# Optimization experiments

Hardware: AMD Instinct MI355X
Metric: run time of the kernel (lower is better)

The kernel has to match this reference:

```python
import jax, jax.numpy as jnp
import numpy as np

EPS = 1e-5
GROUPS = 8
HEADS = 8


def setup_inputs() -> dict:
    key = jax.random.key(0)
    k_x, k_qkv, k_out = jax.random.split(key, 3)
    B, C, X, Y, Z = 2, 256, 16, 16, 16
    x = jax.random.normal(k_x, (B, C, X, Y, Z), dtype=jnp.float32)
    norm_w = jnp.ones((C,), dtype=jnp.float32)
    norm_b = jnp.zeros((C,), dtype=jnp.float32)
    # 1x1 Conv3d weights stored as [out_ch, in_ch]
    w_qkv = jax.random.normal(k_qkv, (3 * C, C), dtype=jnp.float32) * (C ** -0.5)
    w_out = jax.random.normal(k_out, (C, C), dtype=jnp.float32) * (C ** -0.5)
    b_out = jnp.zeros((C,), dtype=jnp.float32)
    return {"x": x, "norm_w": norm_w, "norm_b": norm_b,
            "w_qkv": w_qkv, "w_out": w_out, "b_out": b_out}


def group_norm(x, w, b):
    B, C, X, Y, Z = x.shape
    xg = x.reshape(B, GROUPS, C // GROUPS, X, Y, Z)
    mean = xg.mean(axis=(2, 3, 4, 5), keepdims=True)
    var = xg.var(axis=(2, 3, 4, 5), keepdims=True)
    xn = ((xg - mean) * jax.lax.rsqrt(var + EPS)).reshape(B, C, X, Y, Z)
    return xn * w[None, :, None, None, None] + b[None, :, None, None, None]


def reference(x, norm_w, norm_b, w_qkv, w_out, b_out):
    B, C, X, Y, Z = x.shape
    H = HEADS
    D = C // H
    N = X * Y * Z
    scale = D ** -0.5

    xn = group_norm(x, norm_w, norm_b)
    # 1x1 conv QKV projection (bias=False): [B, 3C, X, Y, Z] flattened to tokens
    qkv = jnp.einsum('oc,bcn->bon', w_qkv, xn.reshape(B, C, N))
    q, k, v = jnp.split(qkv, 3, axis=1)            # each [B, C, N]
    q = q.reshape(B, H, D, N)
    k = k.reshape(B, H, D, N)
    v = v.reshape(B, H, D, N)

    scores = jnp.einsum('bhds,bhdt->bhst', q, k) * scale   # [B, H, N, N]
    probs = jax.nn.softmax(scores, axis=-1)
    out = jnp.einsum('bhst,bhdt->bhds', probs, v)          # [B, H, D, N]
    out = out.reshape(B, C, N)

    # 1x1 conv output projection (with bias)
    out = jnp.einsum('oc,bcn->bon', w_out, out) + b_out[None, :, None]
    return out.reshape(B, C, X, Y, Z) + x
```

## Files before the change

kernel.cpp:

```cpp
#include <hip/hip_runtime.h>

#define NB 2
#define NC 256
#define NT 4096
#define NG 8
#define NH 8
#define EPSV 1e-5f
#define SCALE_L2E 0.25503164427f
#define NCHUNK 4
#define CHTOK (NT / NCHUNK)
#define NIT (CHTOK / 32)
#define PO_ELEMS ((size_t)NB * NC * NT)

typedef __attribute__((ext_vector_type(8))) __bf16 bf16x8;
typedef __attribute__((ext_vector_type(8))) unsigned short u16x8;
typedef __attribute__((ext_vector_type(4))) unsigned short u16x4;
typedef __attribute__((ext_vector_type(4))) unsigned int u32x4;
typedef __attribute__((ext_vector_type(2))) unsigned int u32x2;
typedef __attribute__((ext_vector_type(4))) float f32x4;

static __device__ __forceinline__ unsigned short f2bf(float f) {
    union { float f; unsigned int u; } v; v.f = f;
    unsigned int r = v.u + 0x7fffu + ((v.u >> 16) & 1u);
    return (unsigned short)(r >> 16);
}
static __device__ __forceinline__ float bf2f(unsigned short u) {
    union { unsigned int u; float f; } v; v.u = ((unsigned int)u) << 16;
    return v.f;
}
static __device__ __forceinline__ bf16x8 ldbf8(const unsigned short* p) {
    u16x8 u = *(const u16x8*)p;
    return __builtin_bit_cast(bf16x8, u);
}
static __device__ __forceinline__ unsigned int cvtpk(float lo, float hi) {
    unsigned int d;
    asm("v_cvt_pk_bf16_f32 %0, %1, %2" : "=v"(d) : "v"(lo), "v"(hi));
    return d;
}

__global__ __launch_bounds__(256) void k_stats_partial(const float* __restrict__ x,
                                                       float* __restrict__ part) {
    int bg = blockIdx.x >> 5;
    int p  = blockIdx.x & 31;
    const float4* base = (const float4*)(x + (size_t)bg * 131072 + (size_t)p * 4096);
    float s = 0.f, s2 = 0.f;
#pragma unroll
    for (int i = 0; i < 4; ++i) {
        float4 v = base[threadIdx.x + i * 256];
        s  += v.x + v.y + v.z + v.w;
        s2 += v.x * v.x + v.y * v.y + v.z * v.z + v.w * v.w;
    }
    __shared__ float ss[256], sq[256];
    ss[threadIdx.x] = s; sq[threadIdx.x] = s2;
    __syncthreads();
    for (int off = 128; off > 0; off >>= 1) {
        if (threadIdx.x < off) {
            ss[threadIdx.x] += ss[threadIdx.x + off];
            sq[threadIdx.x] += sq[threadIdx.x + off];
        }
        __syncthreads();
    }
    if (threadIdx.x == 0) {
        part[blockIdx.x * 2 + 0] = ss[0];
        part[blockIdx.x * 2 + 1] = sq[0];
    }
}

__global__ __launch_bounds__(64) void k_stats_final(const float* __restrict__ part,
                                                    float* __restrict__ stats) {
    int bg = blockIdx.x;
    float s = 0.f, s2 = 0.f;
    if (threadIdx.x < 32) {
        s  = part[(bg * 32 + threadIdx.x) * 2 + 0];
        s2 = part[(bg * 32 + threadIdx.x) * 2 + 1];
    }
#pragma unroll
    for (int off = 16; off > 0; off >>= 1) {
        s  += __shfl_down(s, off);
        s2 += __shfl_down(s2, off);
    }
    if (threadIdx.x == 0) {
        const float inv = 1.0f / 131072.0f;
        float mean = s * inv;
        float var  = s2 * inv - mean * mean;
        stats[bg * 2 + 0] = mean;
        stats[bg * 2 + 1] = rsqrtf(var + EPSV);
    }
}

__global__ __launch_bounds__(256) void k_wprep2(const float* __restrict__ wq,
                                                const float* __restrict__ wo,
                                                unsigned short* __restrict__ wq_bf,
                                                unsigned short* __restrict__ wo_bf) {
    int bidx = blockIdx.x;
    const float* src;
    unsigned short* dst;
    int off;
    if (bidx < 96) { src = wq; dst = wq_bf; off = bidx * 2048; }
    else           { src = wo; dst = wo_bf; off = (bidx - 96) * 2048; }
    int idx = off + threadIdx.x * 8;
    float4 a = *(const float4*)(src + idx);
    float4 c = *(const float4*)(src + idx + 4);
    u32x4 o = { cvtpk(a.x, a.y), cvtpk(a.z, a.w),
                cvtpk(c.x, c.y), cvtpk(c.z, c.w) };
    *(u32x4*)(dst + idx) = o;
}

__global__ __launch_bounds__(256) void k_xprep(const float* __restrict__ x,
                                               const float* __restrict__ nw,
                                               const float* __restrict__ nbias,
                                               const float* __restrict__ stats,
                                               unsigned short* __restrict__ xnT) {
    __shared__ unsigned short T[64][72];
    int b = blockIdx.z, c0 = blockIdx.y * 64, n0 = blockIdx.x * 64;
    int tid = threadIdx.x;
    int c_l = tid >> 2, nq = (tid & 3) * 16;
    int c = c0 + c_l;
    int grp = c >> 5;
    float mean = stats[(b * NG + grp) * 2 + 0];
    float rstd = stats[(b * NG + grp) * 2 + 1];
    float wsc = nw[c] * rstd;
    float bb  = nbias[c] - mean * wsc;
    const float4* src = (const float4*)(x + ((size_t)(b * NC + c)) * NT + n0 + nq);
#pragma unroll
    for (int i = 0; i < 4; ++i) {
        float4 v = src[i];
        T[nq + i * 4 + 0][c_l] = f2bf(v.x * wsc + bb);
        T[nq + i * 4 + 1][c_l] = f2bf(v.y * wsc + bb);
        T[nq + i * 4 + 2][c_l] = f2bf(v.z * wsc + bb);
        T[nq + i * 4 + 3][c_l] = f2bf(v.w * wsc + bb);
    }
    __syncthreads();
    int n_l = tid >> 2, cq = (tid & 3) * 16;
    unsigned short* dst = xnT + ((size_t)b * NT + n0 + n_l) * 256 + c0 + cq;
    *(u16x8*)dst       = *(const u16x8*)&T[n_l][cq];
    *(u16x8*)(dst + 8) = *(const u16x8*)&T[n_l][cq + 8];
}

__global__ __launch_bounds__(256) void k_qkv_mfma(const unsigned short* __restrict__ wq_bf,
                                                  const unsigned short* __restrict__ xnT,
                                                  unsigned short* __restrict__ qkT,
                                                  unsigned short* __restrict__ vbf) {
    int b = blockIdx.z, o0 = blockIdx.y * 64, n0 = blockIdx.x * 64;
    int tid = threadIdx.x;
    int w = tid >> 6, lane = tid & 63, c16 = lane & 15, g = lane >> 4;
    int n_tok = n0 + w * 16 + c16;
    const unsigned short* Bsrc = xnT + ((size_t)b * NT + n_tok) * 256 + g * 8;
    const unsigned short* Asrc = wq_bf + (size_t)(o0 + c16) * 256 + g * 8;
    f32x4 acc[4] = {};
    for (int kk = 0; kk < 8; ++kk) {
        bf16x8 bfr = ldbf8(Bsrc + kk * 32);
#pragma unroll
        for (int ot = 0; ot < 4; ++ot) {
            bf16x8 afr = ldbf8(Asrc + ot * 16 * 256 + kk * 32);
            acc[ot] = __builtin_amdgcn_mfma_f32_16x16x32_bf16(afr, bfr, acc[ot], 0, 0, 0);
        }
    }
    if (o0 < 512) {
        int qk = o0 >> 8;
        float sc = (qk == 0) ? SCALE_L2E : 1.0f;
#pragma unroll
        for (int ot = 0; ot < 4; ++ot) {
            int ob = o0 + ot * 16 + g * 4;
            int h  = (ob >> 5) & 7;
            int d4 = ob & 31;
            unsigned int u0 = cvtpk(acc[ot][0] * sc, acc[ot][1] * sc);
            unsigned int u1 = cvtpk(acc[ot][2] * sc, acc[ot][3] * sc);
            u16x4 pk = { (unsigned short)(u0 & 0xFFFF), (unsigned short)(u0 >> 16),
                         (unsigned short)(u1 & 0xFFFF), (unsigned short)(u1 >> 16) };
            *(u16x4*)(qkT + ((((size_t)qk * NB + b) * NH + h) * NT + n_tok) * 32 + d4) = pk;
        }
    } else {
#pragma unroll
        for (int ot = 0; ot < 4; ++ot) {
            int ob = (o0 - 512) + ot * 16 + g * 4;
            int h = (ob >> 5) & 7;
            int d = ob & 31;
            unsigned short* dst = vbf + (((size_t)b * NH + h) * 32 + d) * NT + n_tok;
            dst[0]      = f2bf(acc[ot][0]);
            dst[NT]     = f2bf(acc[ot][1]);
            dst[2 * NT] = f2bf(acc[ot][2]);
            dst[3 * NT] = f2bf(acc[ot][3]);
        }
    }
}

__global__ __launch_bounds__(256) void k_attn(const unsigned short* __restrict__ qkT,
                                              const unsigned short* __restrict__ vbf,
                                              unsigned short* __restrict__ pO,
                                              float* __restrict__ pl) {
    __shared__ unsigned short KV[2048];
    __shared__ unsigned int Pd[4][640];
    int bid = blockIdx.x;
    int xcd  = bid & 7;
    int slot = bid >> 3;
    int combo = xcd * 8 + (slot >> 5);
    int sb    = slot & 31;
    int b  = combo >> 5;
    int ch = (combo >> 3) & 3;
    int h  = combo & 7;

    int tid = threadIdx.x;
    int w = tid >> 6, lane = tid & 63, col = lane & 15, g = lane >> 4;
    int s0 = sb * 128 + w * 32;

    const unsigned short* qB = qkT + ((((size_t)0 * NB + b) * NH + h) * NT) * 32;
    const unsigned short* kB = qkT + ((((size_t)1 * NB + b) * NH + h) * NT) * 32;
    const unsigned short* vB = vbf + (((size_t)b * NH + h) * 32) * NT;

    bf16x8 qf[2];
    qf[0] = ldbf8(qB + (size_t)(s0 + col) * 32 + g * 8);
    qf[1] = ldbf8(qB + (size_t)(s0 + 16 + col) * 32 + g * 8);

    u16x8 ou;
#pragma unroll
    for (int j = 0; j < 8; ++j) ou[j] = 0x3F80;
    const bf16x8 ones = __builtin_bit_cast(bf16x8, ou);

    const unsigned short* gs;
    int gstep;
    if (tid < 128) {
        gs = kB + ((size_t)ch * CHTOK) * 32 + tid * 8;
        gstep = 1024;
    } else {
        int idx = tid - 128;
        int d = idx >> 2, tq = (idx & 3) * 8;
        gs = vB + (size_t)d * NT + ch * CHTOK + tq;
        gstep = 32;
    }

    f32x4 oacc[2][2] = {};
    f32x4 lacc[2] = {};
    unsigned int* Pw = Pd[w];

    u16x8 stg = *(const u16x8*)gs;

    for (int it = 0; it < NIT; ++it) {
        __syncthreads();
        *(u16x8*)&KV[tid * 8] = stg;
        __syncthreads();
        if (it + 1 < NIT)
            stg = *(const u16x8*)(gs + (size_t)(it + 1) * gstep);
        bf16x8 k0 = ldbf8(&KV[0] + col * 32 + g * 8);
        bf16x8 k1 = ldbf8(&KV[0] + (16 + col) * 32 + g * 8);
        bf16x8 v0 = ldbf8(&KV[0] + 1024 + col * 32 + g * 8);
        bf16x8 v1 = ldbf8(&KV[0] + 1024 + (16 + col) * 32 + g * 8);
        const f32x4 z = {0.f, 0.f, 0.f, 0.f};
#pragma unroll
        for (int st = 0; st < 2; ++st) {
            int s_l = st * 16 + col;
            f32x4 sa = __builtin_amdgcn_mfma_f32_16x16x32_bf16(k0, qf[st], z, 0, 0, 0);
            f32x4 sb2 = __builtin_amdgcn_mfma_f32_16x16x32_bf16(k1, qf[st], z, 0, 0, 0);
            unsigned int W0 = cvtpk(__builtin_amdgcn_exp2f(sa[0]),
                                    __builtin_amdgcn_exp2f(sa[1]));
            unsigned int W1 = cvtpk(__builtin_amdgcn_exp2f(sa[2]),
                                    __builtin_amdgcn_exp2f(sa[3]));
            unsigned int W2 = cvtpk(__builtin_amdgcn_exp2f(sb2[0]),
                                    __builtin_amdgcn_exp2f(sb2[1]));
            unsigned int W3 = cvtpk(__builtin_amdgcn_exp2f(sb2[2]),
                                    __builtin_amdgcn_exp2f(sb2[3]));
            u32x2 wlo = {W0, W1};
            u32x2 whi = {W2, W3};
            *(u32x2*)&Pw[s_l * 20 + g * 2]     = wlo;
            *(u32x2*)&Pw[s_l * 20 + 8 + g * 2] = whi;
            u32x4 rv = *(const u32x4*)&Pw[s_l * 20 + g * 4];
            bf16x8 pf = __builtin_bit_cast(bf16x8, rv);
            lacc[st]    = __builtin_amdgcn_mfma_f32_16x16x32_bf16(ones, pf, lacc[st], 0, 0, 0);
            oacc[0][st] = __builtin_amdgcn_mfma_f32_16x16x32_bf16(v0, pf, oacc[0][st], 0, 0, 0);
            oacc[1][st] = __builtin_amdgcn_mfma_f32_16x16x32_bf16(v1, pf, oacc[1][st], 0, 0, 0);
        }
    }

    unsigned short* pOc = pO + (size_t)ch * PO_ELEMS;
#pragma unroll
    for (int dt = 0; dt < 2; ++dt)
#pragma unroll
        for (int st = 0; st < 2; ++st) {
            int s = s0 + st * 16 + col;
            unsigned int u0 = cvtpk(oacc[dt][st][0], oacc[dt][st][1]);
            unsigned int u1 = cvtpk(oacc[dt][st][2], oacc[dt][st][3]);
            u16x4 pk = { (unsigned short)(u0 & 0xFFFF), (unsigned short)(u0 >> 16),
                         (unsigned short)(u1 & 0xFFFF), (unsigned short)(u1 >> 16) };
            *(u16x4*)&pOc[((size_t)(b * NT + s)) * 256 + h * 32 + dt * 16 + g * 4] = pk;
        }
    if (g == 0) {
#pragma unroll
        for (int st = 0; st < 2; ++st) {
            int s = s0 + st * 16 + col;
            pl[(((size_t)ch * NB + b) * NH + h) * NT + s] = lacc[st][0];
        }
    }
}

__global__ __launch_bounds__(512) void k_out_fused(const unsigned short* __restrict__ pO,
                                                   const float* __restrict__ pl,
                                                   const unsigned short* __restrict__ wo_bf,
                                                   const float* __restrict__ bout,
                                                   const float* __restrict__ x,
                                                   float* __restrict__ out) {
    __shared__ unsigned short attL[32 * 264];
    int b = blockIdx.y, n0 = blockIdx.x * 32;
    int tid = threadIdx.x;

#pragma unroll
    for (int i = 0; i < 4; ++i) {
        int q = tid * 4 + i;
        int tok_l = q >> 6;
        int cq = (q & 63) * 4;
        int h = cq >> 5;
        int s = n0 + tok_l;
        float num[4] = {0.f, 0.f, 0.f, 0.f};
        float den = 0.f;
#pragma unroll
        for (int chn = 0; chn < NCHUNK; ++chn) {
            u16x4 ov = *(const u16x4*)&pO[(size_t)chn * PO_ELEMS +
                                          ((size_t)(b * NT + s)) * 256 + cq];
            den += pl[(((size_t)chn * NB + b) * NH + h) * NT + s];
            num[0] += bf2f(ov[0]); num[1] += bf2f(ov[1]);
            num[2] += bf2f(ov[2]); num[3] += bf2f(ov[3]);
        }
        float rd = 1.0f / den;
        u16x4 res = { f2bf(num[0] * rd), f2bf(num[1] * rd),
                      f2bf(num[2] * rd), f2bf(num[3] * rd) };
        *(u16x4*)&attL[tok_l * 264 + cq] = res;
    }
    __syncthreads();

    int w = tid >> 6, lane = tid & 63, c16 = lane & 15, g = lane >> 4;
    int tg = w & 1, og = w >> 1;
    int n_tok = n0 + tg * 16 + c16;
    int o0 = og * 64;
    const unsigned short* Bsrc = &attL[(tg * 16 + c16) * 264 + g * 8];
    const unsigned short* Asrc = wo_bf + (size_t)(o0 + c16) * 256 + g * 8;
    f32x4 acc[4] = {};
    for (int kk = 0; kk < 8; ++kk) {
        bf16x8 bfr = ldbf8(Bsrc + kk * 32);
#pragma unroll
        for (int ot = 0; ot < 4; ++ot) {
            bf16x8 afr = ldbf8(Asrc + ot * 16 * 256 + kk * 32);
            acc[ot] = __builtin_amdgcn_mfma_f32_16x16x32_bf16(afr, bfr, acc[ot], 0, 0, 0);
        }
    }
#pragma unroll
    for (int ot = 0; ot < 4; ++ot) {
        int ob = o0 + ot * 16 + g * 4;
#pragma unroll
        for (int rr = 0; rr < 4; ++rr) {
            int o = ob + rr;
            size_t off = ((size_t)(b * NC + o)) * NT + n_tok;
            out[off] = acc[ot][rr] + bout[o] + x[off];
        }
    }
}

extern "C" void kernel_launch(void* const* d_in, const int* in_sizes, int n_in,
                              void* d_out, int out_size, void* d_ws, size_t ws_size,
                              hipStream_t stream) {
    const float* x    = (const float*)d_in[0];
    const float* nw   = (const float*)d_in[1];
    const float* nb   = (const float*)d_in[2];
    const float* wqkv = (const float*)d_in[3];
    const float* wout = (const float*)d_in[4];
    const float* bout = (const float*)d_in[5];
    float* out = (float*)d_out;
    char* wsb = (char*)d_ws;

    unsigned short* qkT = (unsigned short*)wsb;
    unsigned short* vbf = (unsigned short*)(wsb + 8u * 1024 * 1024);
    unsigned short* pO  = (unsigned short*)(wsb + 12u * 1024 * 1024);
    float* pl   = (float*)(wsb + 28u * 1024 * 1024);
    float* part = (float*)(wsb + 29u * 1024 * 1024);
    float* stats = part + 1024;
    unsigned short* wo_bf = (unsigned short*)(wsb + 30u * 1024 * 1024);
    unsigned short* xnT   = pO;
    unsigned short* wq_bf = (unsigned short*)(wsb + 16u * 1024 * 1024);

    k_stats_partial<<<512, 256, 0, stream>>>(x, part);
    k_stats_final<<<16, 64, 0, stream>>>(part, stats);
    k_wprep2<<<128, 256, 0, stream>>>(wqkv, wout, wq_bf, wo_bf);
    k_xprep<<<dim3(NT / 64, NC / 64, NB), 256, 0, stream>>>(x, nw, nb, stats, xnT);
    k_qkv_mfma<<<dim3(NT / 64, 12, NB), 256, 0, stream>>>(wq_bf, xnT, qkT, vbf);
    k_attn<<<dim3(NB * NCHUNK * NH * 32), 256, 0, stream>>>(qkT, vbf, pO, pl);
    k_out_fused<<<dim3(128, NB), 512, 0, stream>>>(pO, pl, wo_bf, bout, x, out);
}
```

Measured before the change: 121.5 us.

## Keep softmax probabilities in registers by permuting V layout; pad LDS rows

Removes the per-wave LDS round trip that reshuffled the exp'd score fragments into MFMA B-operand layout. Instead, V is loaded from global in two 4-token halves and stored into LDS so its k-index ordering matches the score accumulator register layout, letting the packed probabilities feed the PV MFMA directly. K and V rows in LDS are padded to a stride of 40 to reduce bank conflicts. The register prefetch of the next tile is dropped, so global loads are no longer overlapped with compute, and V global loads become narrower 8-byte accesses.

```diff
diff --git a/kernel.cpp b/kernel.cpp
--- a/kernel.cpp
+++ b/kernel.cpp
@@ -189,8 +189,7 @@
                                               const unsigned short* __restrict__ vbf,
                                               unsigned short* __restrict__ pO,
                                               float* __restrict__ pl) {
-    __shared__ unsigned short KV[2048];
-    __shared__ unsigned int Pd[4][640];
+    __shared__ unsigned short KV[2560];
     int bid = blockIdx.x;
     int xcd  = bid & 7;
     int slot = bid >> 3;
@@ -217,38 +216,43 @@
     for (int j = 0; j < 8; ++j) ou[j] = 0x3F80;
     const bf16x8 ones = __builtin_bit_cast(bf16x8, ou);
 
-    const unsigned short* gs;
-    int gstep;
+    const unsigned short* gsK = kB;
+    const unsigned short* gsVA = vB;
+    const unsigned short* gsVB = vB;
+    int ldst = 0;
     if (tid < 128) {
-        gs = kB + ((size_t)ch * CHTOK) * 32 + tid * 8;
-        gstep = 1024;
+        gsK  = kB + ((size_t)ch * CHTOK) * 32 + tid * 8;
+        ldst = (tid >> 2) * 40 + (tid & 3) * 8;
     } else {
         int idx = tid - 128;
-        int d = idx >> 2, tq = (idx & 3) * 8;
-        gs = vB + (size_t)d * NT + ch * CHTOK + tq;
-        gstep = 32;
+        int d = idx >> 2, q = idx & 3;
+        gsVA = vB + (size_t)d * NT + ch * CHTOK + q * 4;
+        gsVB = gsVA + 16;
+        ldst = 1280 + d * 40 + q * 8;
     }
 
     f32x4 oacc[2][2] = {};
     f32x4 lacc[2] = {};
-    unsigned int* Pw = Pd[w];
-
-    u16x8 stg = *(const u16x8*)gs;
 
     for (int it = 0; it < NIT; ++it) {
         __syncthreads();
-        *(u16x8*)&KV[tid * 8] = stg;
+        if (tid < 128) {
+            *(u16x8*)&KV[ldst] = *(const u16x8*)(gsK + (size_t)it * 1024);
+        } else {
+            u16x4 va4 = *(const u16x4*)(gsVA + it * 32);
+            u16x4 vb4 = *(const u16x4*)(gsVB + it * 32);
+            u16x8 vv = { va4[0], va4[1], va4[2], va4[3],
+                         vb4[0], vb4[1], vb4[2], vb4[3] };
+            *(u16x8*)&KV[ldst] = vv;
+        }
         __syncthreads();
-        if (it + 1 < NIT)
-            stg = *(const u16x8*)(gs + (size_t)(it + 1) * gstep);
-        bf16x8 k0 = ldbf8(&KV[0] + col * 32 + g * 8);
-        bf16x8 k1 = ldbf8(&KV[0] + (16 + col) * 32 + g * 8);
-        bf16x8 v0 = ldbf8(&KV[0] + 1024 + col * 32 + g * 8);
-        bf16x8 v1 = ldbf8(&KV[0] + 1024 + (16 + col) * 32 + g * 8);
+        bf16x8 k0 = ldbf8(&KV[col * 40 + g * 8]);
+        bf16x8 k1 = ldbf8(&KV[(16 + col) * 40 + g * 8]);
+        bf16x8 v0 = ldbf8(&KV[1280 + col * 40 + g * 8]);
+        bf16x8 v1 = ldbf8(&KV[1280 + (16 + col) * 40 + g * 8]);
         const f32x4 z = {0.f, 0.f, 0.f, 0.f};
 #pragma unroll
         for (int st = 0; st < 2; ++st) {
-            int s_l = st * 16 + col;
             f32x4 sa = __builtin_amdgcn_mfma_f32_16x16x32_bf16(k0, qf[st], z, 0, 0, 0);
             f32x4 sb2 = __builtin_amdgcn_mfma_f32_16x16x32_bf16(k1, qf[st], z, 0, 0, 0);
             unsigned int W0 = cvtpk(__builtin_amdgcn_exp2f(sa[0]),
@@ -259,12 +263,8 @@
                                     __builtin_amdgcn_exp2f(sb2[1]));
             unsigned int W3 = cvtpk(__builtin_amdgcn_exp2f(sb2[2]),
                                     __builtin_amdgcn_exp2f(sb2[3]));
-            u32x2 wlo = {W0, W1};
-            u32x2 whi = {W2, W3};
-            *(u32x2*)&Pw[s_l * 20 + g * 2]     = wlo;
-            *(u32x2*)&Pw[s_l * 20 + 8 + g * 2] = whi;
-            u32x4 rv = *(const u32x4*)&Pw[s_l * 20 + g * 4];
-            bf16x8 pf = __builtin_bit_cast(bf16x8, rv);
+            u32x4 pbw = {W0, W1, W2, W3};
+            bf16x8 pf = __builtin_bit_cast(bf16x8, pbw);
             lacc[st]    = __builtin_amdgcn_mfma_f32_16x16x32_bf16(ones, pf, lacc[st], 0, 0, 0);
             oacc[0][st] = __builtin_amdgcn_mfma_f32_16x16x32_bf16(v0, pf, oacc[0][st], 0, 0, 0);
             oacc[1][st] = __builtin_amdgcn_mfma_f32_16x16x32_bf16(v1, pf, oacc[1][st], 0, 0, 0);
```

After: 113.3 us (median of 2 runs). 1.07x faster.
